# Performance work log

Hardware: AMD Instinct MI355X
Metric: run time of the kernel (lower is better)

The kernel has to match this reference:

```python
import jax, jax.numpy as jnp
import numpy as np

BOUND = 5.0
MIN_D = 1e-3
MIN_BW = 1e-3
MIN_BH = 1e-3
EPS = 1e-8
B, F, K = 131072, 256, 16


def setup_inputs() -> dict:
    key = jax.random.key(0)
    k1, k2, k3, k4 = jax.random.split(key, 4)
    return {
        "x": jax.random.normal(k1, (B, F), dtype=jnp.float32),
        "uw": jax.random.normal(k2, (F, K), dtype=jnp.float32),
        "uh": jax.random.normal(k3, (F, K), dtype=jnp.float32),
        "ud": jax.random.normal(k4, (F, K - 1), dtype=jnp.float32),
        "input_shift": jnp.zeros((F,), dtype=jnp.float32),
        "input_scale": jnp.ones((F,), dtype=jnp.float32),
    }


def _knots(u, mb):
    # u: [F, K] unnormalized bin sizes -> knot positions [F, K+1] and sizes [F, K]
    f, k = u.shape
    w = jax.nn.softmax(u, axis=-1)
    w = mb + (1.0 - mb * k) * w
    c = jnp.concatenate([jnp.zeros((f, 1), u.dtype), jnp.cumsum(w, axis=-1)], axis=-1)
    c = 2.0 * BOUND * c - BOUND
    c = c.at[:, 0].set(-BOUND).at[:, -1].set(BOUND)
    return c, c[:, 1:] - c[:, :-1]


def reference(x, uw, uh, ud, input_shift, input_scale):
    f, k = uw.shape
    # normalize input to spline domain
    xn = (x - input_shift[None, :]) / input_scale[None, :]

    # knot positions / bin sizes
    cw, w = _knots(uw, MIN_BW)   # [F, K+1], [F, K]
    ch, h = _knots(uh, MIN_BH)

    # derivatives at knots; boundaries padded so derivative = 1 (linear tails)
    const = float(np.log(np.expm1(1.0 - MIN_D)))
    pad = jnp.full((f, 1), const, dtype=ud.dtype)
    d = MIN_D + jax.nn.softplus(jnp.concatenate([pad, ud, pad], axis=-1))  # [F, K+1]

    inside = (xn > -BOUND) & (xn < BOUND)
    xc = jnp.clip(xn, -BOUND, BOUND)

    # per-feature bucketize: searchsorted over each feature's knots
    idx = jax.vmap(lambda a, v: jnp.searchsorted(a, v, side="right"),
                   in_axes=(0, 1), out_axes=1)(cw, xc) - 1  # [B, F]
    idx = jnp.clip(idx, 0, k - 1)

    fa = jnp.arange(f)[None, :]
    icw = cw[fa, idx]   # left knot x
    ibw = w[fa, idx]    # bin width
    ich = ch[fa, idx]   # left knot y
    ibh = h[fa, idx]    # bin height
    delta = ibh / ibw
    d0 = d[fa, idx]
    d1 = d[fa, idx + 1]

    # rational-quadratic evaluation
    theta = (xc - icw) / ibw
    t1m = theta * (1.0 - theta)
    numer = ibh * (delta * theta * theta + d0 * t1m)
    denom = delta + (d0 + d1 - 2.0 * delta) * t1m
    s = jnp.where(inside, ich + numer / denom, xn)  # identity linear tails

    # gauge fix: standardize per feature with batch stats (biased var)
    mean = jnp.mean(s, axis=0)
    var = jnp.mean((s - mean[None, :]) ** 2, axis=0)
    z = (s - mean[None, :]) / jnp.sqrt(var[None, :] + EPS)
    return z
```

## Files before the change

### kernel.cpp

```cpp
#include <hip/hip_runtime.h>
#include <math.h>


#define FEAT 256
#define KBINS 16
#define BATCH 131072
#define BOUNDF 5.0f
#define MIN_Df 1e-3f
#define MIN_BWf 1e-3f
#define MIN_BHf 1e-3f
#define EPSF 1e-8f

#define FTB 32
#define FT_TILES 8
#define SLOTB 8
#define RBB 256
#define ROWS_PB (BATCH / RBB)
#define ITERB (ROWS_PB / SLOTB)

#define R_P0   0
#define R_P1   17408
#define R_CW   34816
#define R_MEAN 39168
#define R_ISTD 39424
#define R_PS   39680
#define R_PS2  (R_PS + 2048 * 32)
#define TAB_FLOATS (R_PS2 + 2048 * 32)
#define S_ELEMS ((size_t)BATCH * FEAT)
#define S_FLOATS (S_ELEMS / 2)

__device__ __forceinline__ unsigned short f2bf(float x) {
    unsigned int b = __float_as_uint(x);
    unsigned int r = (b + 0x7fffu + ((b >> 16) & 1u)) >> 16;
    return (unsigned short)r;
}

__global__ __launch_bounds__(256) void k_params(const float* __restrict__ uw,
                                                const float* __restrict__ uh,
                                                const float* __restrict__ ud,
                                                float* __restrict__ tab) {
    int f = threadIdx.x;
    float cw[17], ch[17], dv[17];
    {
        float u[KBINS];
#pragma unroll
        for (int j = 0; j < KBINS; j++) u[j] = uw[f * KBINS + j];
        float m = u[0];
#pragma unroll
        for (int j = 1; j < KBINS; j++) m = fmaxf(m, u[j]);
        float ssum = 0.f;
#pragma unroll
        for (int j = 0; j < KBINS; j++) { u[j] = expf(u[j] - m); ssum += u[j]; }
        float inv = 1.0f / ssum;
        float cum = 0.f;
        cw[0] = -BOUNDF;
#pragma unroll
        for (int j = 1; j < KBINS; j++) {
            float wj = MIN_BWf + (1.0f - MIN_BWf * (float)KBINS) * (u[j - 1] * inv);
            cum += wj;
            cw[j] = 2.0f * BOUNDF * cum - BOUNDF;
        }
        cw[KBINS] = BOUNDF;
    }
    {
        float u[KBINS];
#pragma unroll
        for (int j = 0; j < KBINS; j++) u[j] = uh[f * KBINS + j];
        float m = u[0];
#pragma unroll
        for (int j = 1; j < KBINS; j++) m = fmaxf(m, u[j]);
        float ssum = 0.f;
#pragma unroll
        for (int j = 0; j < KBINS; j++) { u[j] = expf(u[j] - m); ssum += u[j]; }
        float inv = 1.0f / ssum;
        float cum = 0.f;
        ch[0] = -BOUNDF;
#pragma unroll
        for (int j = 1; j < KBINS; j++) {
            float wj = MIN_BHf + (1.0f - MIN_BHf * (float)KBINS) * (u[j - 1] * inv);
            cum += wj;
            ch[j] = 2.0f * BOUNDF * cum - BOUNDF;
        }
        ch[KBINS] = BOUNDF;
    }
    {
        dv[0] = 1.0f;
        dv[KBINS] = 1.0f;
#pragma unroll
        for (int j = 1; j < KBINS; j++) {
            float v = ud[f * (KBINS - 1) + (j - 1)];
            float sp = fmaxf(v, 0.0f) + log1pf(expf(-fabsf(v)));
            dv[j] = MIN_Df + sp;
        }
    }
#pragma unroll
    for (int j = 0; j <= KBINS; j++) tab[R_CW + f * 17 + j] = cw[j];
    float4* P0g = (float4*)(tab + R_P0);
    float4* P1g = (float4*)(tab + R_P1);
#pragma unroll
    for (int i = 0; i < KBINS; i++) {
        float w = cw[i + 1] - cw[i];
        float binv = 1.0f / w;
        float hb = ch[i + 1] - ch[i];
        float delta = hb * binv;
        float4 p0, p1;
        p0.x = cw[i] * binv;
        p0.y = binv;
        p0.z = hb * delta;
        p0.w = hb * dv[i];
        p1.x = dv[i] + dv[i + 1] - 2.0f * delta;
        p1.y = delta;
        p1.z = ch[i];
        p1.w = 0.0f;
        P0g[f * 17 + i] = p0;
        P1g[f * 17 + i] = p1;
    }
}

__device__ __forceinline__ float eval_rq(float xv, float a, float nb,
                                         const float4* __restrict__ sP0,
                                         const float4* __restrict__ sP1,
                                         const float kn[15], int l17) {
    float xn = fmaf(xv, a, nb);
    float xc = fminf(fmaxf(xn, -BOUNDF), BOUNDF);
    int idx = 0;
#pragma unroll
    for (int j = 0; j < 15; j++) idx += (xc >= kn[j]) ? 1 : 0;
    int o = l17 + idx;
    float4 p0 = sP0[o];
    float4 p1 = sP1[o];
    float th = fmaf(xc, p0.y, -p0.x);
    float th2 = th * th;
    float t1m = th - th2;
    float numer = fmaf(p0.z, th2, p0.w * t1m);
    float denom = fmaf(p1.x, t1m, p1.y);
    float s = fmaf(numer, __builtin_amdgcn_rcpf(denom), p1.z);
    return (fabsf(xn) < BOUNDF) ? s : xn;
}

template <bool STORE_S>
__global__ __launch_bounds__(256, 6) void k_pass1(const float* __restrict__ X,
                                                  const float* __restrict__ shiftp,
                                                  const float* __restrict__ scalep,
                                                  float* __restrict__ tab,
                                                  unsigned short* __restrict__ S) {
    __shared__ float4 sP0[FTB * 17];
    __shared__ float4 sP1[FTB * 17];
    __shared__ float red[2][SLOTB][FTB];
    int t = threadIdx.x;
    int rb = blockIdx.x, ft = blockIdx.y;
    const float4* P0g = (const float4*)(tab + R_P0) + ft * FTB * 17;
    const float4* P1g = (const float4*)(tab + R_P1) + ft * FTB * 17;
    for (int i = t; i < FTB * 17; i += 256) { sP0[i] = P0g[i]; sP1[i] = P1g[i]; }
    int l = t & 31, slot = t >> 5;
    int f = ft * FTB + l;
    float kn[15];
#pragma unroll
    for (int j = 0; j < 15; j++) kn[j] = tab[R_CW + f * 17 + 1 + j];
    float a = 1.0f / scalep[f];
    float nb = -shiftp[f] * a;
    int l17 = l * 17;
    __syncthreads();
    size_t base = (size_t)(rb * ROWS_PB + slot) * FEAT + f;
    const float* Xp = X + base;
    unsigned short* Sp = STORE_S ? (S + base) : nullptr;
    float sum = 0.f, sumsq = 0.f;
    for (int r = 0; r < ITERB; r += 4) {
        float x0 = Xp[0 * SLOTB * FEAT];
        float x1 = Xp[1 * SLOTB * FEAT];
        float x2 = Xp[2 * SLOTB * FEAT];
        float x3 = Xp[3 * SLOTB * FEAT];
        Xp += 4 * SLOTB * FEAT;
        float s0 = eval_rq(x0, a, nb, sP0, sP1, kn, l17);
        float s1 = eval_rq(x1, a, nb, sP0, sP1, kn, l17);
        float s2 = eval_rq(x2, a, nb, sP0, sP1, kn, l17);
        float s3 = eval_rq(x3, a, nb, sP0, sP1, kn, l17);
        if (STORE_S) {
            Sp[0 * SLOTB * FEAT] = f2bf(s0);
            Sp[1 * SLOTB * FEAT] = f2bf(s1);
            Sp[2 * SLOTB * FEAT] = f2bf(s2);
            Sp[3 * SLOTB * FEAT] = f2bf(s3);
            Sp += 4 * SLOTB * FEAT;
        }
        sum += s0; sumsq = fmaf(s0, s0, sumsq);
        sum += s1; sumsq = fmaf(s1, s1, sumsq);
        sum += s2; sumsq = fmaf(s2, s2, sumsq);
        sum += s3; sumsq = fmaf(s3, s3, sumsq);
    }
    red[0][slot][l] = sum;
    red[1][slot][l] = sumsq;
    __syncthreads();
    if (t < FTB) {
        float v = 0.f;
#pragma unroll
        for (int s2i = 0; s2i < SLOTB; s2i++) v += red[0][s2i][t];
        tab[R_PS + (ft * RBB + rb) * FTB + t] = v;
    } else if (t < 2 * FTB) {
        int u = t - FTB;
        float v = 0.f;
#pragma unroll
        for (int s2i = 0; s2i < SLOTB; s2i++) v += red[1][s2i][u];
        tab[R_PS2 + (ft * RBB + rb) * FTB + u] = v;
    }
}

__global__ __launch_bounds__(256) void k_reduce(float* __restrict__ tab) {
    int f = blockIdx.x;
    int ft = f >> 5, l = f & 31;
    int t = threadIdx.x;
    __shared__ float r1[256], r2[256];
    r1[t] = tab[R_PS + (ft * RBB + t) * FTB + l];
    r2[t] = tab[R_PS2 + (ft * RBB + t) * FTB + l];
    __syncthreads();
    for (int off = 128; off > 0; off >>= 1) {
        if (t < off) { r1[t] += r1[t + off]; r2[t] += r2[t + off]; }
        __syncthreads();
    }
    if (t == 0) {
        float mean = r1[0] * (1.0f / (float)BATCH);
        float var = r2[0] * (1.0f / (float)BATCH) - mean * mean;
        var = fmaxf(var, 0.0f);
        tab[R_MEAN + f] = mean;
        tab[R_ISTD + f] = 1.0f / sqrtf(var + EPSF);
    }
}

__global__ __launch_bounds__(256, 8) void k_pass2_stream(const unsigned short* __restrict__ S,
                                                         const float* __restrict__ tab,
                                                         float* __restrict__ Z) {
    int gid = blockIdx.x * 256 + threadIdx.x;
    int fg = gid & 31;
    int rs = gid >> 5;
    const float* meanp = tab + R_MEAN + fg * 8;
    const float* istdp = tab + R_ISTD + fg * 8;
    float istd[8], nmi[8];
#pragma unroll
    for (int j = 0; j < 8; j++) {
        float m = meanp[j];
        float is = istdp[j];
        istd[j] = is;
        nmi[j] = -m * is;
    }
    size_t idx = (size_t)rs * 8 * FEAT + fg * 8;
#pragma unroll
    for (int r = 0; r < 8; r++) {
        uint4 sv = *(const uint4*)(S + idx);
        float z0 = fmaf(__uint_as_float((sv.x & 0xffffu) << 16), istd[0], nmi[0]);
        float z1 = fmaf(__uint_as_float(sv.x & 0xffff0000u),     istd[1], nmi[1]);
        float z2 = fmaf(__uint_as_float((sv.y & 0xffffu) << 16), istd[2], nmi[2]);
        float z3 = fmaf(__uint_as_float(sv.y & 0xffff0000u),     istd[3], nmi[3]);
        float z4 = fmaf(__uint_as_float((sv.z & 0xffffu) << 16), istd[4], nmi[4]);
        float z5 = fmaf(__uint_as_float(sv.z & 0xffff0000u),     istd[5], nmi[5]);
        float z6 = fmaf(__uint_as_float((sv.w & 0xffffu) << 16), istd[6], nmi[6]);
        float z7 = fmaf(__uint_as_float(sv.w & 0xffff0000u),     istd[7], nmi[7]);
        float4* Zp = (float4*)(Z + idx);
        Zp[0] = make_float4(z0, z1, z2, z3);
        Zp[1] = make_float4(z4, z5, z6, z7);
        idx += FEAT;
    }
}

__global__ __launch_bounds__(256, 6) void k_pass2_eval(const float* __restrict__ X,
                                                       const float* __restrict__ shiftp,
                                                       const float* __restrict__ scalep,
                                                       const float* __restrict__ tab,
                                                       float* __restrict__ Z) {
    __shared__ float4 sP0[FTB * 17];
    __shared__ float4 sP1[FTB * 17];
    int t = threadIdx.x;
    int rb = blockIdx.x, ft = blockIdx.y;
    const float4* P0g = (const float4*)(tab + R_P0) + ft * FTB * 17;
    const float4* P1g = (const float4*)(tab + R_P1) + ft * FTB * 17;
    for (int i = t; i < FTB * 17; i += 256) { sP0[i] = P0g[i]; sP1[i] = P1g[i]; }
    int l = t & 31, slot = t >> 5;
    int f = ft * FTB + l;
    float kn[15];
#pragma unroll
    for (int j = 0; j < 15; j++) kn[j] = tab[R_CW + f * 17 + 1 + j];
    float a = 1.0f / scalep[f];
    float nb = -shiftp[f] * a;
    float mean = tab[R_MEAN + f];
    float istd = tab[R_ISTD + f];
    int l17 = l * 17;
    __syncthreads();
    size_t base = (size_t)(rb * ROWS_PB + slot) * FEAT + f;
    const float* Xp = X + base;
    float* Zp = Z + base;
    for (int r = 0; r < ITERB; r += 4) {
        float x0 = Xp[0 * SLOTB * FEAT];
        float x1 = Xp[1 * SLOTB * FEAT];
        float x2 = Xp[2 * SLOTB * FEAT];
        float x3 = Xp[3 * SLOTB * FEAT];
        Xp += 4 * SLOTB * FEAT;
        float s0 = eval_rq(x0, a, nb, sP0, sP1, kn, l17);
        float s1 = eval_rq(x1, a, nb, sP0, sP1, kn, l17);
        float s2 = eval_rq(x2, a, nb, sP0, sP1, kn, l17);
        float s3 = eval_rq(x3, a, nb, sP0, sP1, kn, l17);
        Zp[0 * SLOTB * FEAT] = (s0 - mean) * istd;
        Zp[1 * SLOTB * FEAT] = (s1 - mean) * istd;
        Zp[2 * SLOTB * FEAT] = (s2 - mean) * istd;
        Zp[3 * SLOTB * FEAT] = (s3 - mean) * istd;
        Zp += 4 * SLOTB * FEAT;
    }
}

extern "C" void kernel_launch(void* const* d_in, const int* in_sizes, int n_in,
                              void* d_out, int out_size, void* d_ws, size_t ws_size,
                              hipStream_t stream) {
    const float* x     = (const float*)d_in[0];
    const float* uw    = (const float*)d_in[1];
    const float* uh    = (const float*)d_in[2];
    const float* ud    = (const float*)d_in[3];
    const float* shift = (const float*)d_in[4];
    const float* scale = (const float*)d_in[5];
    float* out = (float*)d_out;
    float* ws  = (float*)d_ws;

    size_t need = (S_FLOATS + (size_t)TAB_FLOATS) * sizeof(float);
    bool useS = ws_size >= need;
    float* tab = ws + (useS ? S_FLOATS : 0);
    unsigned short* S = (unsigned short*)ws;

    k_params<<<1, 256, 0, stream>>>(uw, uh, ud, tab);
    if (useS) {
        k_pass1<true><<<dim3(RBB, FT_TILES), 256, 0, stream>>>(x, shift, scale, tab, S);
        k_reduce<<<FEAT, 256, 0, stream>>>(tab);
        k_pass2_stream<<<2048, 256, 0, stream>>>(S, tab, out);
    } else {
        k_pass1<false><<<dim3(RBB, FT_TILES), 256, 0, stream>>>(x, shift, scale, tab, nullptr);
        k_reduce<<<FEAT, 256, 0, stream>>>(tab);
        k_pass2_eval<<<dim3(RBB, FT_TILES), 256, 0, stream>>>(x, shift, scale, tab, out);
    }
}
```

Measured before the change: 114.3 us.

## Use branchless binary search and bin-major LDS table layout for spline eval

Replaces the 15-compare linear count used for bucketing with a 4-level branchless binary search over the knots held in registers, and drops the clamp because out-of-range values take the identity path anyway. The parameter tables move from a feature-major stride-17 layout to a bin-major layout, so LDS indexing becomes (bin<<5)|lane, and the knot table is stored transposed so its global loads coalesce. Launch-bounds occupancy rises from 6 to 8 blocks per SM. The select chains may cost about as much ALU as the compares they replace, and the higher occupancy target can force register spills.

```diff
diff --git a/kernel.cpp b/kernel.cpp
--- a/kernel.cpp
+++ b/kernel.cpp
@@ -19,11 +19,11 @@
 #define ITERB (ROWS_PB / SLOTB)
 
 #define R_P0   0
-#define R_P1   17408
-#define R_CW   34816
-#define R_MEAN 39168
-#define R_ISTD 39424
-#define R_PS   39680
+#define R_P1   16384
+#define R_KN   32768
+#define R_MEAN 36864
+#define R_ISTD 37120
+#define R_PS   37376
 #define R_PS2  (R_PS + 2048 * 32)
 #define TAB_FLOATS (R_PS2 + 2048 * 32)
 #define S_ELEMS ((size_t)BATCH * FEAT)
@@ -94,7 +94,7 @@
         }
     }
 #pragma unroll
-    for (int j = 0; j <= KBINS; j++) tab[R_CW + f * 17 + j] = cw[j];
+    for (int j = 0; j < 15; j++) tab[R_KN + j * 256 + f] = cw[j + 1];
     float4* P0g = (float4*)(tab + R_P0);
     float4* P1g = (float4*)(tab + R_P1);
 #pragma unroll
@@ -112,24 +112,29 @@
         p1.y = delta;
         p1.z = ch[i];
         p1.w = 0.0f;
-        P0g[f * 17 + i] = p0;
-        P1g[f * 17 + i] = p1;
+        P0g[i * 256 + f] = p0;
+        P1g[i * 256 + f] = p1;
     }
 }
 
 __device__ __forceinline__ float eval_rq(float xv, float a, float nb,
                                          const float4* __restrict__ sP0,
                                          const float4* __restrict__ sP1,
-                                         const float kn[15], int l17) {
+                                         const float kn[15], int l) {
     float xn = fmaf(xv, a, nb);
-    float xc = fminf(fmaxf(xn, -BOUNDF), BOUNDF);
-    int idx = 0;
-#pragma unroll
-    for (int j = 0; j < 15; j++) idx += (xc >= kn[j]) ? 1 : 0;
-    int o = l17 + idx;
+    bool c3 = xn >= kn[7];
+    float p2 = c3 ? kn[11] : kn[3];
+    bool c2 = xn >= p2;
+    float p1v = c3 ? (c2 ? kn[13] : kn[9]) : (c2 ? kn[5] : kn[1]);
+    bool c1 = xn >= p1v;
+    float p0v = c3 ? (c2 ? (c1 ? kn[14] : kn[12]) : (c1 ? kn[10] : kn[8]))
+                   : (c2 ? (c1 ? kn[6] : kn[4]) : (c1 ? kn[2] : kn[0]));
+    bool c0 = xn >= p0v;
+    int idx = ((int)c3 << 3) | ((int)c2 << 2) | ((int)c1 << 1) | (int)c0;
+    int o = (idx << 5) | l;
     float4 p0 = sP0[o];
     float4 p1 = sP1[o];
-    float th = fmaf(xc, p0.y, -p0.x);
+    float th = fmaf(xn, p0.y, -p0.x);
     float th2 = th * th;
     float t1m = th - th2;
     float numer = fmaf(p0.z, th2, p0.w * t1m);
@@ -139,27 +144,30 @@
 }
 
 template <bool STORE_S>
-__global__ __launch_bounds__(256, 6) void k_pass1(const float* __restrict__ X,
+__global__ __launch_bounds__(256, 8) void k_pass1(const float* __restrict__ X,
                                                   const float* __restrict__ shiftp,
                                                   const float* __restrict__ scalep,
                                                   float* __restrict__ tab,
                                                   unsigned short* __restrict__ S) {
-    __shared__ float4 sP0[FTB * 17];
-    __shared__ float4 sP1[FTB * 17];
+    __shared__ float4 sP0[16 * FTB];
+    __shared__ float4 sP1[16 * FTB];
     __shared__ float red[2][SLOTB][FTB];
     int t = threadIdx.x;
     int rb = blockIdx.x, ft = blockIdx.y;
-    const float4* P0g = (const float4*)(tab + R_P0) + ft * FTB * 17;
-    const float4* P1g = (const float4*)(tab + R_P1) + ft * FTB * 17;
-    for (int i = t; i < FTB * 17; i += 256) { sP0[i] = P0g[i]; sP1[i] = P1g[i]; }
+    const float4* P0g = (const float4*)(tab + R_P0);
+    const float4* P1g = (const float4*)(tab + R_P1);
+    for (int s = t; s < 16 * FTB; s += 256) {
+        int bin = s >> 5, li = s & 31;
+        sP0[s] = P0g[bin * 256 + ft * FTB + li];
+        sP1[s] = P1g[bin * 256 + ft * FTB + li];
+    }
     int l = t & 31, slot = t >> 5;
     int f = ft * FTB + l;
     float kn[15];
 #pragma unroll
-    for (int j = 0; j < 15; j++) kn[j] = tab[R_CW + f * 17 + 1 + j];
+    for (int j = 0; j < 15; j++) kn[j] = tab[R_KN + j * 256 + f];
     float a = 1.0f / scalep[f];
     float nb = -shiftp[f] * a;
-    int l17 = l * 17;
     __syncthreads();
     size_t base = (size_t)(rb * ROWS_PB + slot) * FEAT + f;
     const float* Xp = X + base;
@@ -171,10 +179,10 @@
         float x2 = Xp[2 * SLOTB * FEAT];
         float x3 = Xp[3 * SLOTB * FEAT];
         Xp += 4 * SLOTB * FEAT;
-        float s0 = eval_rq(x0, a, nb, sP0, sP1, kn, l17);
-        float s1 = eval_rq(x1, a, nb, sP0, sP1, kn, l17);
-        float s2 = eval_rq(x2, a, nb, sP0, sP1, kn, l17);
-        float s3 = eval_rq(x3, a, nb, sP0, sP1, kn, l17);
+        float s0 = eval_rq(x0, a, nb, sP0, sP1, kn, l);
+        float s1 = eval_rq(x1, a, nb, sP0, sP1, kn, l);
+        float s2 = eval_rq(x2, a, nb, sP0, sP1, kn, l);
+        float s3 = eval_rq(x3, a, nb, sP0, sP1, kn, l);
         if (STORE_S) {
             Sp[0 * SLOTB * FEAT] = f2bf(s0);
             Sp[1 * SLOTB * FEAT] = f2bf(s1);
@@ -260,28 +268,31 @@
     }
 }
 
-__global__ __launch_bounds__(256, 6) void k_pass2_eval(const float* __restrict__ X,
+__global__ __launch_bounds__(256, 8) void k_pass2_eval(const float* __restrict__ X,
                                                        const float* __restrict__ shiftp,
                                                        const float* __restrict__ scalep,
                                                        const float* __restrict__ tab,
                                                        float* __restrict__ Z) {
-    __shared__ float4 sP0[FTB * 17];
-    __shared__ float4 sP1[FTB * 17];
+    __shared__ float4 sP0[16 * FTB];
+    __shared__ float4 sP1[16 * FTB];
     int t = threadIdx.x;
     int rb = blockIdx.x, ft = blockIdx.y;
-    const float4* P0g = (const float4*)(tab + R_P0) + ft * FTB * 17;
-    const float4* P1g = (const float4*)(tab + R_P1) + ft * FTB * 17;
-    for (int i = t; i < FTB * 17; i += 256) { sP0[i] = P0g[i]; sP1[i] = P1g[i]; }
+    const float4* P0g = (const float4*)(tab + R_P0);
+    const float4* P1g = (const float4*)(tab + R_P1);
+    for (int s = t; s < 16 * FTB; s += 256) {
+        int bin = s >> 5, li = s & 31;
+        sP0[s] = P0g[bin * 256 + ft * FTB + li];
+        sP1[s] = P1g[bin * 256 + ft * FTB + li];
+    }
     int l = t & 31, slot = t >> 5;
     int f = ft * FTB + l;
     float kn[15];
 #pragma unroll
-    for (int j = 0; j < 15; j++) kn[j] = tab[R_CW + f * 17 + 1 + j];
+    for (int j = 0; j < 15; j++) kn[j] = tab[R_KN + j * 256 + f];
     float a = 1.0f / scalep[f];
     float nb = -shiftp[f] * a;
     float mean = tab[R_MEAN + f];
     float istd = tab[R_ISTD + f];
-    int l17 = l * 17;
     __syncthreads();
     size_t base = (size_t)(rb * ROWS_PB + slot) * FEAT + f;
     const float* Xp = X + base;
@@ -292,10 +303,10 @@
         float x2 = Xp[2 * SLOTB * FEAT];
         float x3 = Xp[3 * SLOTB * FEAT];
         Xp += 4 * SLOTB * FEAT;
-        float s0 = eval_rq(x0, a, nb, sP0, sP1, kn, l17);
-        float s1 = eval_rq(x1, a, nb, sP0, sP1, kn, l17);
-        float s2 = eval_rq(x2, a, nb, sP0, sP1, kn, l17);
-        float s3 = eval_rq(x3, a, nb, sP0, sP1, kn, l17);
+        float s0 = eval_rq(x0, a, nb, sP0, sP1, kn, l);
+        float s1 = eval_rq(x1, a, nb, sP0, sP1, kn, l);
+        float s2 = eval_rq(x2, a, nb, sP0, sP1, kn, l);
+        float s3 = eval_rq(x3, a, nb, sP0, sP1, kn, l);
         Zp[0 * SLOTB * FEAT] = (s0 - mean) * istd;
         Zp[1 * SLOTB * FEAT] = (s1 - mean) * istd;
         Zp[2 * SLOTB * FEAT] = (s2 - mean) * istd;
```

Result: slower. 204.7 us (+79.1%).
